# Kernel tuning notes

Measured on AMD Instinct MI355X. Metric: run time of the kernel, lower is better.

## Reference

```python
import jax, jax.numpy as jnp
import numpy as np

NUM_CAMS = 6
H_IMG, W_IMG = 256, 256
H_MAP, W_MAP = 64, 64
BS, N_JOINTS = 64, 20


def _compute_kp_coords(heatmap):
    # heatmap: [N, J, h_map, w_map], N = bs*num_cams
    N, J = heatmap.shape[:2]
    h = heatmap * 100.0
    flat = h.reshape(N, J, -1)
    flat = jax.nn.softmax(flat, axis=2)
    confidence = jnp.max(flat, axis=2) / jnp.sum(flat, axis=2)  # [N, J]
    hm = flat.reshape(N, J, H_MAP, W_MAP)
    mass_x = hm.sum(axis=2)  # [N, J, W] (sum over rows)
    mass_y = hm.sum(axis=3)  # [N, J, H] (sum over cols)
    x = (mass_x * jnp.arange(W_MAP, dtype=hm.dtype)).sum(axis=2)  # [N, J]
    y = (mass_y * jnp.arange(H_MAP, dtype=hm.dtype)).sum(axis=2)  # [N, J]
    kp_2d_heatmap = jnp.stack([x, y, confidence], axis=-1)  # [N, J, 3]
    # NOTE: original code scales x by h_img/h_map and y by w_img/w_map (kept faithful)
    kp_2d_croped = jnp.stack([x * (H_IMG / H_MAP), y * (W_IMG / W_MAP), confidence], axis=-1)
    return kp_2d_heatmap, kp_2d_croped


def _forward(heatmap, proj_matrices, confidences):
    kp_2d_heatmap, kp_2d_croped = _compute_kp_coords(heatmap)
    J = kp_2d_croped.shape[1]
    kpc = kp_2d_croped.reshape(BS, NUM_CAMS, J, 3)
    kph = kp_2d_heatmap.reshape(BS, NUM_CAMS, J, 3)
    conf = confidences.reshape(BS, NUM_CAMS, J)
    conf = conf / conf.sum(axis=1, keepdims=True) + 1e-5

    pts = kpc[..., :2]                    # [B, C, J, 2]
    row2 = proj_matrices[:, :, 2]         # [B, C, 4]
    # A[b,c,j] = P_row2 * (x,y)^T - P_rows01, weighted by confidence
    A = row2[:, :, None, None, :] * pts[..., None] - proj_matrices[:, :, None, :2, :]  # [B,C,J,2,4]
    A = A * conf[..., None, None]
    A = A.transpose(0, 2, 1, 3, 4).reshape(BS, J, 2 * NUM_CAMS, 4)  # [B, J, 2C, 4]

    # batched SVD of tiny 12x4 matrices; last right singular vector spans null space
    _, _, vh = jnp.linalg.svd(A, full_matrices=False)  # vh: [B, J, 4, 4]
    homo = -vh[..., 3, :]                               # [B, J, 4]
    kp_3d = homo[..., :3] / homo[..., 3:4]
    res_triang = jnp.abs(jnp.einsum('bjnk,bjk->bjn', A, homo)).sum(axis=-1)  # L1 residual
    return kp_3d, res_triang, kpc, kph


def setup_inputs() -> dict:
    key = jax.random.key(0)
    k1, k2, k3 = jax.random.split(key, 3)
    heatmap = jax.random.normal(k1, (BS * NUM_CAMS, N_JOINTS, H_MAP, W_MAP), dtype=jnp.float32)
    proj_matrices = jax.random.normal(k2, (BS, NUM_CAMS, 3, 4), dtype=jnp.float32)
    confidences = jax.random.uniform(k3, (BS * NUM_CAMS, N_JOINTS), dtype=jnp.float32)
    return {"heatmap": heatmap, "proj_matrices": proj_matrices, "confidences": confidences}


def reference(heatmap, proj_matrices, confidences):
    return _forward(heatmap, proj_matrices, confidences)
```

## Files before the change

kernel.cpp:

```cpp
#include <hip/hip_runtime.h>
#include <math.h>

#define NMAPS   7680
#define BSZ     64
#define NCAMS   6
#define NJ      20

#define OFF_KP3D 0
#define OFF_RES  3840
#define OFF_KPC  5120
#define OFF_KPH  28160

typedef float floatx4 __attribute__((ext_vector_type(4)));

__device__ __forceinline__ float waveMax(float v) {
#pragma unroll
    for (int off = 32; off > 0; off >>= 1)
        v = fmaxf(v, __shfl_down(v, off, 64));
    return v;
}

__device__ __forceinline__ double waveSum(double v) {
#pragma unroll
    for (int off = 32; off > 0; off >>= 1)
        v += __shfl_down(v, off, 64);
    return v;
}

__global__ __launch_bounds__(256) void kp_kernel(const float* __restrict__ hm,
                                                 float* __restrict__ out) {
    const int b = blockIdx.x;
    const int t = threadIdx.x;
    const floatx4* base = (const floatx4*)(hm + (size_t)b * 4096);

    floatx4 v[4];
#pragma unroll
    for (int i = 0; i < 4; i++) v[i] = __builtin_nontemporal_load(&base[t + 256 * i]);

    float m = v[0].x;
#pragma unroll
    for (int i = 0; i < 4; i++)
        m = fmaxf(m, fmaxf(fmaxf(v[i].x, v[i].y), fmaxf(v[i].z, v[i].w)));

    __shared__ float  smax[4];
    __shared__ double sred[3][4];
    const int wave = t >> 6, lane = t & 63;

    float wm = waveMax(m);
    if (lane == 0) smax[wave] = wm;
    __syncthreads();
    const float gmax = fmaxf(fmaxf(smax[0], smax[1]), fmaxf(smax[2], smax[3]));
    const float hmax = 100.0f * gmax;

    double se = 0.0, sx = 0.0, sy = 0.0;
#pragma unroll
    for (int i = 0; i < 4; i++) {
        const int idx0 = (t + 256 * i) * 4;
        const float vals[4] = {v[i].x, v[i].y, v[i].z, v[i].w};
#pragma unroll
        for (int k = 0; k < 4; k++) {
            const float e = expf(100.0f * vals[k] - hmax);
            const int idx = idx0 + k;
            se += (double)e;
            sx += (double)e * (double)(idx & 63);
            sy += (double)e * (double)(idx >> 6);
        }
    }
    se = waveSum(se); sx = waveSum(sx); sy = waveSum(sy);
    if (lane == 0) { sred[0][wave] = se; sred[1][wave] = sx; sred[2][wave] = sy; }
    __syncthreads();

    if (t == 0) {
        const double SE = sred[0][0] + sred[0][1] + sred[0][2] + sred[0][3];
        const double SX = sred[1][0] + sred[1][1] + sred[1][2] + sred[1][3];
        const double SY = sred[2][0] + sred[2][1] + sred[2][2] + sred[2][3];
        const float x    = (float)(SX / SE);
        const float y    = (float)(SY / SE);
        const float conf = (float)(1.0 / SE);
        const int o = b * 3;
        out[OFF_KPH + o + 0] = x;
        out[OFF_KPH + o + 1] = y;
        out[OFF_KPH + o + 2] = conf;
        out[OFF_KPC + o + 0] = 4.0f * x;
        out[OFF_KPC + o + 1] = 4.0f * y;
        out[OFF_KPC + o + 2] = conf;
    }
}

__global__ __launch_bounds__(256) void tri_kernel(const float* __restrict__ proj,
                                                  const float* __restrict__ confin,
                                                  float* __restrict__ out) {
    const int t = blockIdx.x * blockDim.x + threadIdx.x;
    if (t >= BSZ * NJ) return;
    const int bs = t / NJ, j = t % NJ;

    float cn[NCAMS];
    float csum = 0.0f;
#pragma unroll
    for (int c = 0; c < NCAMS; c++) {
        cn[c] = confin[(bs * NCAMS + c) * NJ + j];
        csum += cn[c];
    }
#pragma unroll
    for (int c = 0; c < NCAMS; c++) cn[c] = cn[c] / csum + 1e-5f;

    float A[12][4];
#pragma unroll
    for (int c = 0; c < NCAMS; c++) {
        const float* P = proj + ((size_t)bs * NCAMS + c) * 12;
        const int kidx = OFF_KPC + ((bs * NCAMS + c) * NJ + j) * 3;
        const float px = out[kidx + 0];
        const float py = out[kidx + 1];
#pragma unroll
        for (int k = 0; k < 4; k++) {
            const float r2 = P[8 + k];
            A[c * 2 + 0][k] = (r2 * px - P[k])     * cn[c];
            A[c * 2 + 1][k] = (r2 * py - P[4 + k]) * cn[c];
        }
    }

    double M[4][4], V[4][4];
    double diagmax = 0.0;
#pragma unroll
    for (int a = 0; a < 4; a++)
#pragma unroll
        for (int b2 = a; b2 < 4; b2++) {
            double s = 0.0;
#pragma unroll
            for (int n = 0; n < 12; n++) s += (double)A[n][a] * (double)A[n][b2];
            M[a][b2] = s; M[b2][a] = s;
            if (a == b2) diagmax = fmax(diagmax, fabs(s));
        }
#pragma unroll
    for (int a = 0; a < 4; a++)
#pragma unroll
        for (int b2 = 0; b2 < 4; b2++) V[a][b2] = (a == b2) ? 1.0 : 0.0;

    const double skip_tol = diagmax * 1e-18;
    for (int sweep = 0; sweep < 6; sweep++) {
#pragma unroll
        for (int p = 0; p < 3; p++)
#pragma unroll
            for (int q2 = p + 1; q2 < 4; q2++) {
                const double apq = M[p][q2];
                if (fabs(apq) <= skip_tol) continue;
                const double tau = (M[q2][q2] - M[p][p]) / (2.0 * apq);
                const double tt  = (tau >= 0.0 ? 1.0 : -1.0) /
                                   (fabs(tau) + sqrt(1.0 + tau * tau));
                const double c   = 1.0 / sqrt(1.0 + tt * tt);
                const double s   = tt * c;
#pragma unroll
                for (int k = 0; k < 4; k++) {
                    const double mkp = M[k][p], mkq = M[k][q2];
                    M[k][p]  = c * mkp - s * mkq;
                    M[k][q2] = s * mkp + c * mkq;
                }
#pragma unroll
                for (int k = 0; k < 4; k++) {
                    const double mpk = M[p][k], mqk = M[q2][k];
                    M[p][k]  = c * mpk - s * mqk;
                    M[q2][k] = s * mpk + c * mqk;
                }
#pragma unroll
                for (int k = 0; k < 4; k++) {
                    const double vkp = V[k][p], vkq = V[k][q2];
                    V[k][p]  = c * vkp - s * vkq;
                    V[k][q2] = s * vkp + c * vkq;
                }
            }
    }

    int mi = 0;
#pragma unroll
    for (int i = 1; i < 4; i++)
        if (M[i][i] < M[mi][mi]) mi = i;
    const double h0 = V[0][mi], h1 = V[1][mi], h2 = V[2][mi], h3 = V[3][mi];

    out[OFF_KP3D + t * 3 + 0] = (float)(h0 / h3);
    out[OFF_KP3D + t * 3 + 1] = (float)(h1 / h3);
    out[OFF_KP3D + t * 3 + 2] = (float)(h2 / h3);

    const float hf0 = (float)h0, hf1 = (float)h1, hf2 = (float)h2, hf3 = (float)h3;
    float res = 0.0f;
#pragma unroll
    for (int n = 0; n < 12; n++)
        res += fabsf(A[n][0] * hf0 + A[n][1] * hf1 + A[n][2] * hf2 + A[n][3] * hf3);
    out[OFF_RES + t] = res;
}

extern "C" void kernel_launch(void* const* d_in, const int* in_sizes, int n_in,
                              void* d_out, int out_size, void* d_ws, size_t ws_size,
                              hipStream_t stream) {
    const float* heatmap = (const float*)d_in[0];
    const float* proj    = (const float*)d_in[1];
    const float* confid  = (const float*)d_in[2];
    float* out = (float*)d_out;

    hipLaunchKernelGGL(kp_kernel, dim3(NMAPS), dim3(256), 0, stream, heatmap, out);
    hipLaunchKernelGGL(tri_kernel, dim3((BSZ * NJ + 255) / 256), dim3(256), 0, stream,
                       proj, confid, out);
}
```

Before: 196.2 us.

## Map one heatmap per wavefront and reduce in float with factored moments

The keypoint kernel now gives each 64-lane wavefront a whole heatmap, so the shared-memory reductions and block barriers go away. Each lane holds 64 values. Exponentials use the fast __expf intrinsic and are accumulated per component in float. The x and y moments are rebuilt from per-lane partial sums in double before a butterfly shuffle reduction. Nontemporal loads are dropped, and the triangulation kernel is launched with 64-thread blocks to spread its 1280 threads over more CUs. The changes trade some accuracy (float accumulation and approximate exp) and higher register use for fewer double-precision operations and no synchronization.

```diff
diff --git a/kernel.cpp b/kernel.cpp
--- a/kernel.cpp
+++ b/kernel.cpp
@@ -13,71 +13,56 @@
 
 typedef float floatx4 __attribute__((ext_vector_type(4)));
 
-__device__ __forceinline__ float waveMax(float v) {
-#pragma unroll
-    for (int off = 32; off > 0; off >>= 1)
-        v = fmaxf(v, __shfl_down(v, off, 64));
-    return v;
-}
-
-__device__ __forceinline__ double waveSum(double v) {
-#pragma unroll
-    for (int off = 32; off > 0; off >>= 1)
-        v += __shfl_down(v, off, 64);
-    return v;
-}
-
 __global__ __launch_bounds__(256) void kp_kernel(const float* __restrict__ hm,
                                                  float* __restrict__ out) {
-    const int b = blockIdx.x;
-    const int t = threadIdx.x;
-    const floatx4* base = (const floatx4*)(hm + (size_t)b * 4096);
+    const int wave = threadIdx.x >> 6;
+    const int lane = threadIdx.x & 63;
+    const int map  = blockIdx.x * 4 + wave;
+    const floatx4* base = (const floatx4*)(hm + (size_t)map * 4096);
 
-    floatx4 v[4];
+    floatx4 v[16];
 #pragma unroll
-    for (int i = 0; i < 4; i++) v[i] = __builtin_nontemporal_load(&base[t + 256 * i]);
+    for (int i = 0; i < 16; i++) v[i] = base[lane + 64 * i];
 
     float m = v[0].x;
 #pragma unroll
-    for (int i = 0; i < 4; i++)
+    for (int i = 0; i < 16; i++)
         m = fmaxf(m, fmaxf(fmaxf(v[i].x, v[i].y), fmaxf(v[i].z, v[i].w)));
+#pragma unroll
+    for (int off = 32; off > 0; off >>= 1)
+        m = fmaxf(m, __shfl_xor(m, off, 64));
+    const float hmax = 100.0f * m;
 
-    __shared__ float  smax[4];
-    __shared__ double sred[3][4];
-    const int wave = t >> 6, lane = t & 63;
+    float ek0 = 0.f, ek1 = 0.f, ek2 = 0.f, ek3 = 0.f;
+    float si  = 0.f;
+#pragma unroll
+    for (int i = 0; i < 16; i++) {
+        const float e0 = __expf(100.0f * v[i].x - hmax);
+        const float e1 = __expf(100.0f * v[i].y - hmax);
+        const float e2 = __expf(100.0f * v[i].z - hmax);
+        const float e3 = __expf(100.0f * v[i].w - hmax);
+        ek0 += e0; ek1 += e1; ek2 += e2; ek3 += e3;
+        const float se_i = (e0 + e1) + (e2 + e3);
+        si = fmaf((float)i, se_i, si);
+    }
 
-    float wm = waveMax(m);
-    if (lane == 0) smax[wave] = wm;
-    __syncthreads();
-    const float gmax = fmaxf(fmaxf(smax[0], smax[1]), fmaxf(smax[2], smax[3]));
-    const float hmax = 100.0f * gmax;
+    const double dk0 = (double)ek0, dk1 = (double)ek1;
+    const double dk2 = (double)ek2, dk3 = (double)ek3;
+    double se = (dk0 + dk1) + (dk2 + dk3);
+    double sx = (double)(4 * (lane & 15)) * se + (dk1 + 2.0 * dk2 + 3.0 * dk3);
+    double sy = (double)(lane >> 4) * se + 4.0 * (double)si;
+#pragma unroll
+    for (int off = 32; off > 0; off >>= 1) {
+        se += __shfl_xor(se, off, 64);
+        sx += __shfl_xor(sx, off, 64);
+        sy += __shfl_xor(sy, off, 64);
+    }
 
-    double se = 0.0, sx = 0.0, sy = 0.0;
-#pragma unroll
-    for (int i = 0; i < 4; i++) {
-        const int idx0 = (t + 256 * i) * 4;
-        const float vals[4] = {v[i].x, v[i].y, v[i].z, v[i].w};
-#pragma unroll
-        for (int k = 0; k < 4; k++) {
-            const float e = expf(100.0f * vals[k] - hmax);
-            const int idx = idx0 + k;
-            se += (double)e;
-            sx += (double)e * (double)(idx & 63);
-            sy += (double)e * (double)(idx >> 6);
-        }
-    }
-    se = waveSum(se); sx = waveSum(sx); sy = waveSum(sy);
-    if (lane == 0) { sred[0][wave] = se; sred[1][wave] = sx; sred[2][wave] = sy; }
-    __syncthreads();
-
-    if (t == 0) {
-        const double SE = sred[0][0] + sred[0][1] + sred[0][2] + sred[0][3];
-        const double SX = sred[1][0] + sred[1][1] + sred[1][2] + sred[1][3];
-        const double SY = sred[2][0] + sred[2][1] + sred[2][2] + sred[2][3];
-        const float x    = (float)(SX / SE);
-        const float y    = (float)(SY / SE);
-        const float conf = (float)(1.0 / SE);
-        const int o = b * 3;
+    if (lane == 0) {
+        const float x    = (float)(sx / se);
+        const float y    = (float)(sy / se);
+        const float conf = (float)(1.0 / se);
+        const int o = map * 3;
         out[OFF_KPH + o + 0] = x;
         out[OFF_KPH + o + 1] = y;
         out[OFF_KPH + o + 2] = conf;
@@ -87,9 +72,9 @@
     }
 }
 
-__global__ __launch_bounds__(256) void tri_kernel(const float* __restrict__ proj,
-                                                  const float* __restrict__ confin,
-                                                  float* __restrict__ out) {
+__global__ __launch_bounds__(64) void tri_kernel(const float* __restrict__ proj,
+                                                 const float* __restrict__ confin,
+                                                 float* __restrict__ out) {
     const int t = blockIdx.x * blockDim.x + threadIdx.x;
     if (t >= BSZ * NJ) return;
     const int bs = t / NJ, j = t % NJ;
@@ -196,7 +181,7 @@
     const float* confid  = (const float*)d_in[2];
     float* out = (float*)d_out;
 
-    hipLaunchKernelGGL(kp_kernel, dim3(NMAPS), dim3(256), 0, stream, heatmap, out);
-    hipLaunchKernelGGL(tri_kernel, dim3((BSZ * NJ + 255) / 256), dim3(256), 0, stream,
+    hipLaunchKernelGGL(kp_kernel, dim3(NMAPS / 4), dim3(256), 0, stream, heatmap, out);
+    hipLaunchKernelGGL(tri_kernel, dim3((BSZ * NJ + 63) / 64), dim3(64), 0, stream,
                        proj, confid, out);
 }
```

Measured after the change: 198.9 us. Within noise of the previous version (+1.4%).
